# Optimization experiments

Hardware: AMD Instinct MI355X
Metric: run time of the kernel (lower is better)

The kernel has to match this reference:

```python
import jax, jax.numpy as jnp
import numpy as np

T = 8192   # sequence length (= max_seq_len)
E = 1024   # embedding dim
D = 11     # hard-coded projection dim in source


def setup_inputs() -> dict:
    key = jax.random.key(0)
    ks = jax.random.split(key, 6)
    s_e = 1.0 / np.sqrt(E)
    s_d = 1.0 / np.sqrt(D)
    return {
        "x": jax.random.randint(ks[0], (T,), 0, 32000, dtype=jnp.int64),
        "x_embeddings": jax.random.normal(ks[1], (T, E), dtype=jnp.float32),
        "Wk": jax.random.normal(ks[2], (D, E), dtype=jnp.float32) * s_e,
        "bk": jnp.zeros((D,), dtype=jnp.float32),
        "Wq": jax.random.normal(ks[3], (D, E), dtype=jnp.float32) * s_e,
        "bq": jnp.zeros((D,), dtype=jnp.float32),
        "Wv": jax.random.normal(ks[4], (D, E), dtype=jnp.float32) * s_e,
        "bv": jnp.zeros((D,), dtype=jnp.float32),
        "Wf": jax.random.normal(ks[5], (E, D), dtype=jnp.float32) * s_d,
        "bf": jnp.zeros((E,), dtype=jnp.float32),
    }


def reference(x, x_embeddings, Wk, bk, Wq, bq, Wv, bv, Wf, bf):
    t = x.shape[0]  # static under jit
    k = x_embeddings @ Wk.T + bk            # [T, D]
    q = x_embeddings @ Wq.T + bq            # [T, D]
    v = x_embeddings @ Wv.T + bv            # [T, D]
    att = q @ k.T                           # [T, T]; NOTE: no 1/sqrt(D) scaling in source
    causal = jnp.tril(jnp.ones((t, t), dtype=bool))
    att = jnp.where(causal, att, -jnp.inf)
    att = jax.nn.softmax(att, axis=1)       # dim=1 as in source
    res = att @ v                           # [T, D]
    return res @ Wf.T + bf                  # [T, E]
```

## Files before the change

kernel.cpp:

```cpp
#include <hip/hip_runtime.h>

#define T_SEQ 8192
#define E_DIM 1024
#define QS 36
#define QNEC 8
#define QKC 64
#define QX4 16
#define QXST 17
#define QRB 64
#define AJW 16
#define ABJ 64
#define ARB 256
#define KVW 24
#define TR 16

__device__ __forceinline__ float2 pkfma(float2 a, float2 b, float2 c) {
    return make_float2(fmaf(a.x, b.x, c.x), fmaf(a.y, b.y, c.y));
}
__device__ __forceinline__ float2 f2(float x, float y) { return make_float2(x, y); }

__device__ __forceinline__ void pack3s(const float2 o[6], float4* dst) {
    float4 t;
    t.x = o[0].x; t.y = o[0].y; t.z = o[1].x; t.w = o[1].y; dst[0]   = t;
    t.x = o[2].x; t.y = o[2].y; t.z = o[3].x; t.w = o[3].y; dst[64]  = t;
    t.x = o[4].x; t.y = o[4].y; t.z = o[5].x; t.w = o[5].y; dst[128] = t;
}
__device__ __forceinline__ void pack3(const float2 o[6], float4* dst) {
    float4 t;
    t.x = o[0].x; t.y = o[0].y; t.z = o[1].x; t.w = o[1].y; dst[0] = t;
    t.x = o[2].x; t.y = o[2].y; t.z = o[3].x; t.w = o[3].y; dst[1] = t;
    t.x = o[4].x; t.y = o[4].y; t.z = o[5].x; t.w = o[5].y; dst[2] = t;
}
__device__ __forceinline__ void add3s(float2 o[6], const float4* src) {
    float4 s0 = src[0], s1 = src[64], s2 = src[128];
    o[0].x += s0.x; o[0].y += s0.y; o[1].x += s0.z; o[1].y += s0.w;
    o[2].x += s1.x; o[2].y += s1.y; o[3].x += s1.z; o[3].y += s1.w;
    o[4].x += s2.x; o[4].y += s2.y; o[5].x += s2.z; o[5].y += s2.w;
}


__global__ __launch_bounds__(256) void qkv_proj(
    const float* __restrict__ xe,
    const float* __restrict__ Wk, const float* __restrict__ bk,
    const float* __restrict__ Wq, const float* __restrict__ bq,
    const float* __restrict__ Wv, const float* __restrict__ bv,
    float* __restrict__ partQ) {
    const int row0 = blockIdx.x * QRB;
    const int ec = blockIdx.y;
    const int lane = threadIdx.x & 63;
    const int wg = threadIdx.x >> 6;

    __shared__ float4 xT[QRB * QXST];
    __shared__ float4 wT[36 * QX4];

    float2 acc[9];
#pragma unroll
    for (int k = 0; k < 9; ++k) acc[k] = f2(0.f, 0.f);

    for (int cc = 0; cc < 2; ++cc) {
        const int cb = ec * 128 + cc * QKC;
        if (cc) __syncthreads();

#pragma unroll
        for (int t = 0; t < 4; ++t) {
            int idx = threadIdx.x + t * 256;
            int r = idx >> 4, c4 = idx & 15;
            xT[r * QXST + c4] =
                *(const float4*)(xe + (size_t)(row0 + r) * E_DIM + cb + c4 * 4);
        }
        for (int idx = threadIdx.x; idx < 36 * QX4; idx += 256) {
            int r = idx >> 4, c4 = idx & 15;
            float4 v = make_float4(0.f, 0.f, 0.f, 0.f);
            if (r < 33) {
                const float* base = (r < 11) ? (Wk + (size_t)r * E_DIM)
                                  : (r < 22) ? (Wq + (size_t)(r - 11) * E_DIM)
                                             : (Wv + (size_t)(r - 22) * E_DIM);
                v = *(const float4*)(base + cb + c4 * 4);
            }
            wT[idx] = v;
        }
        __syncthreads();

        const float4* xr = xT + lane * QXST;
        const float4* wr = wT + wg * 9 * QX4;
#pragma unroll 4
        for (int c4 = 0; c4 < QX4; ++c4) {
            float4 xv = xr[c4];
#pragma unroll
            for (int k = 0; k < 9; ++k) {
                float4 wv = wr[k * QX4 + c4];
                acc[k] = pkfma(f2(xv.x, xv.y), f2(wv.x, wv.y), acc[k]);
                acc[k] = pkfma(f2(xv.z, xv.w), f2(wv.z, wv.w), acc[k]);
            }
        }
    }

    __syncthreads();
    float* res = (float*)xT;
#pragma unroll
    for (int k = 0; k < 9; ++k) {
        int o = wg * 9 + k;
        bool live = (o < 33);
        int c = (o < 11) ? o : (o < 22) ? o + 1 : (o < 33) ? o + 2
              : (o == 33) ? 11 : (o == 34) ? 23 : 35;
        float b = 0.f;
        if (ec == 0 && live)
            b = (o < 11) ? bk[o] : (o < 22) ? bq[o - 11] : bv[o - 22];
        res[lane * 36 + c] = live ? (acc[k].x + acc[k].y + b) : 0.f;
    }
    __syncthreads();

    float4* dst = (float4*)(partQ + ((size_t)ec * T_SEQ + row0) * QS);
    for (int idx = threadIdx.x; idx < QRB * 9; idx += 256) {
        int r = idx / 9, f = idx % 9;
        dst[idx] = *(const float4*)(res + r * 36 + f * 4);
    }
}

__global__ __launch_bounds__(256) void reduceQ(const float* __restrict__ partQ,
                                               float* __restrict__ qkvF) {
    const size_t idx = (size_t)blockIdx.x * 256 + threadIdx.x;
    const float4* p = (const float4*)partQ;
    const size_t cs = (size_t)T_SEQ * (QS / 4);
    float4 s = make_float4(0.f, 0.f, 0.f, 0.f);
#pragma unroll
    for (int c = 0; c < QNEC; ++c) {
        float4 a = p[idx + (size_t)c * cs];
        s.x += a.x; s.y += a.y; s.z += a.z; s.w += a.w;
    }
    ((float4*)qkvF)[idx] = s;
}

__global__ __launch_bounds__(256) void attn(const float* __restrict__ qkvF,
                                            float* __restrict__ part) {
    const int b = blockIdx.x;
    int rb = 0;
    while (2 * (rb + 1) * (rb + 2) <= b) ++rb;
    const int c = b - 2 * rb * (rb + 1);
    const int lane = threadIdx.x & 63;
    const int wid = threadIdx.x >> 6;
    const int r0 = rb * ARB + lane * 4;
    const int j0 = c * ABJ + wid * AJW;

    __shared__ float sh[3072];
    float* kv = sh + wid * (AJW * KVW);

    float2 q[4][6], o[4][6];
#pragma unroll
    for (int i = 0; i < 4; ++i) {
        const float* qp = qkvF + (size_t)(r0 + i) * QS + 12;
#pragma unroll
        for (int d = 0; d < 5; ++d) q[i][d] = f2(qp[2 * d], qp[2 * d + 1]);
        q[i][5] = f2(qp[10], 0.f);
#pragma unroll
        for (int d = 0; d < 6; ++d) o[i][d] = f2(0.f, 0.f);
    }

#pragma unroll
    for (int t = 0; t < 2; ++t) {
        int idx = lane + t * 64;
        if (idx < AJW * 6) {
            int row = idx / 6, f = idx % 6;
            int srcOff = f * 4 + (f >= 3 ? 12 : 0);
            float4 v = *(const float4*)(qkvF + (size_t)(j0 + row) * QS + srcOff);
            *(float4*)(kv + row * KVW + f * 4) = v;
        }
    }

    for (int jj = 0; jj < AJW; ++jj) {
        const float* kp = kv + jj * KVW;
        const float4 kA = *(const float4*)(kp);
        const float4 kB = *(const float4*)(kp + 4);
        const float4 kC = *(const float4*)(kp + 8);
        const float4 vA = *(const float4*)(kp + 12);
        const float4 vB = *(const float4*)(kp + 16);
        const float4 vC = *(const float4*)(kp + 20);
        const float2 k01 = f2(kA.x, kA.y), k23 = f2(kA.z, kA.w);
        const float2 k45 = f2(kB.x, kB.y), k67 = f2(kB.z, kB.w);
        const float2 k89 = f2(kC.x, kC.y), kXp = f2(kC.z, kC.w);
        const int j = j0 + jj;

#pragma unroll
        for (int i = 0; i < 4; ++i) {
            float2 s = pkfma(q[i][0], k01, pkfma(q[i][1], k23, pkfma(q[i][2], k45,
                       pkfma(q[i][3], k67, pkfma(q[i][4], k89,
                       pkfma(q[i][5], kXp, f2(0.f, 0.f)))))));
            float pe = __expf(s.x + s.y);
            pe = (j <= r0 + i) ? pe : 0.f;
            float2 p2 = f2(pe, pe);
            o[i][0] = pkfma(p2, f2(vA.x, vA.y), o[i][0]);
            o[i][1] = pkfma(p2, f2(vA.z, vA.w), o[i][1]);
            o[i][2] = pkfma(p2, f2(vB.x, vB.y), o[i][2]);
            o[i][3] = pkfma(p2, f2(vB.z, vB.w), o[i][3]);
            o[i][4] = pkfma(p2, f2(vC.x, vC.y), o[i][4]);
            o[i][5] = pkfma(p2, f2(vC.z, 1.f),  o[i][5]);
        }
    }

    float4* buf = (float4*)sh;
    __syncthreads();
    if (wid == 1) {
#pragma unroll
        for (int i = 0; i < 4; ++i) pack3s(o[i], buf + (i * 3) * 64 + lane);
    }
    __syncthreads();
    if (wid == 0) {
#pragma unroll
        for (int i = 0; i < 4; ++i) add3s(o[i], buf + (i * 3) * 64 + lane);
    }
    __syncthreads();
    if (wid == 3) {
#pragma unroll
        for (int i = 0; i < 4; ++i) pack3s(o[i], buf + (i * 3) * 64 + lane);
    }
    __syncthreads();
    if (wid == 2) {
#pragma unroll
        for (int i = 0; i < 4; ++i) add3s(o[i], buf + (i * 3) * 64 + lane);
    }
    __syncthreads();
    if (wid == 2) {
#pragma unroll
        for (int i = 0; i < 4; ++i) pack3s(o[i], buf + (i * 3) * 64 + lane);
    }
    __syncthreads();
    if (wid == 0) {
#pragma unroll
        for (int i = 0; i < 4; ++i) add3s(o[i], buf + (i * 3) * 64 + lane);
        float* d0 = part + ((size_t)c * T_SEQ + r0) * 12;
#pragma unroll
        for (int i = 0; i < 4; ++i) pack3(o[i], (float4*)(d0 + i * 12));
    }
}

__global__ __launch_bounds__(256) void pass2(const float* __restrict__ part,
                                             const float* __restrict__ Wf,
                                             const float* __restrict__ bf,
                                             float* __restrict__ out) {
    const int t0 = blockIdx.x * TR;
    const int cnt = 4 * (t0 / ARB) + 4;
    __shared__ float red[16][16][12];
    __shared__ float res[TR][12];
    {
        const int r = threadIdx.x >> 4;
        const int s = threadIdx.x & 15;
        float a[12];
#pragma unroll
        for (int d = 0; d < 12; ++d) a[d] = 0.f;
        const size_t S = (size_t)T_SEQ * 12;
        const float* p = part + (size_t)(t0 + r) * 12;
        for (int c = s; c < cnt; c += 16) {
            const float4* pc = (const float4*)(p + (size_t)c * S);
            float4 x0 = pc[0], x1 = pc[1], x2 = pc[2];
            a[0] += x0.x; a[1] += x0.y; a[2]  += x0.z; a[3]  += x0.w;
            a[4] += x1.x; a[5] += x1.y; a[6]  += x1.z; a[7]  += x1.w;
            a[8] += x2.x; a[9] += x2.y; a[10] += x2.z; a[11] += x2.w;
        }
#pragma unroll
        for (int d = 0; d < 12; ++d) red[r][s][d] = a[d];
    }
    __syncthreads();
    if (threadIdx.x < TR * 12) {
        const int r = threadIdx.x / 12, d = threadIdx.x % 12;
        float sum = 0.f;
#pragma unroll
        for (int s = 0; s < 16; ++s) sum += red[r][s][d];
        res[r][d] = (d == 11) ? (1.f / sum) : sum;
    }
    __syncthreads();

    const int e0 = threadIdx.x * 4;
    float w[4][11];
    const float* wp = Wf + (size_t)e0 * 11;
#pragma unroll
    for (int ee = 0; ee < 4; ++ee)
#pragma unroll
        for (int i = 0; i < 11; ++i) w[ee][i] = wp[ee * 11 + i];
    const float4 bv = *(const float4*)(bf + e0);

    for (int r = 0; r < TR; ++r) {
        float rr[12];
#pragma unroll
        for (int d = 0; d < 12; ++d) rr[d] = res[r][d];
        float2 a0 = f2(0.f, 0.f), a1 = a0, a2 = a0, a3 = a0;
#pragma unroll
        for (int d = 0; d < 10; d += 2) {
            float2 rv = f2(rr[d], rr[d + 1]);
            a0 = pkfma(rv, f2(w[0][d], w[0][d + 1]), a0);
            a1 = pkfma(rv, f2(w[1][d], w[1][d + 1]), a1);
            a2 = pkfma(rv, f2(w[2][d], w[2][d + 1]), a2);
            a3 = pkfma(rv, f2(w[3][d], w[3][d + 1]), a3);
        }
        const float rl = rr[11];
        float4 ov;
        ov.x = (a0.x + a0.y + rr[10] * w[0][10]) * rl + bv.x;
        ov.y = (a1.x + a1.y + rr[10] * w[1][10]) * rl + bv.y;
        ov.z = (a2.x + a2.y + rr[10] * w[2][10]) * rl + bv.z;
        ov.w = (a3.x + a3.y + rr[10] * w[3][10]) * rl + bv.w;
        *(float4*)(out + (size_t)(t0 + r) * E_DIM + e0) = ov;
    }
}

extern "C" void kernel_launch(void* const* d_in, const int* in_sizes, int n_in,
                              void* d_out, int out_size, void* d_ws, size_t ws_size,
                              hipStream_t stream) {
    const float* xe = (const float*)d_in[1];
    const float* Wk = (const float*)d_in[2];
    const float* bk = (const float*)d_in[3];
    const float* Wq = (const float*)d_in[4];
    const float* bq = (const float*)d_in[5];
    const float* Wv = (const float*)d_in[6];
    const float* bv = (const float*)d_in[7];
    const float* Wf = (const float*)d_in[8];
    const float* bf = (const float*)d_in[9];
    float* out = (float*)d_out;

    float* qkvF  = (float*)d_ws;
    float* partQ = qkvF + (size_t)T_SEQ * QS;
    float* part  = partQ;

    qkv_proj<<<dim3(T_SEQ / QRB, QNEC), 256, 0, stream>>>(xe, Wk, bk, Wq, bq, Wv, bv, partQ);
    reduceQ<<<(T_SEQ * QS / 4) / 256, 256, 0, stream>>>(partQ, qkvF);
    attn<<<2112, 256, 0, stream>>>(qkvF, part);
    pass2<<<T_SEQ / TR, 256, 0, stream>>>(part, Wf, bf, out);
}
```

Before: 163.8 us.

## Fuse Q reduction into projection via last-block atomic and fold final attention row-block

```diff
diff --git a/kernel.cpp b/kernel.cpp
--- a/kernel.cpp
+++ b/kernel.cpp
@@ -44,7 +44,8 @@
     const float* __restrict__ Wk, const float* __restrict__ bk,
     const float* __restrict__ Wq, const float* __restrict__ bq,
     const float* __restrict__ Wv, const float* __restrict__ bv,
-    float* __restrict__ partQ) {
+    float* __restrict__ partQ, float* __restrict__ qkvF,
+    int* __restrict__ cntQ) {
     const int row0 = blockIdx.x * QRB;
     const int ec = blockIdx.y;
     const int lane = threadIdx.x & 63;
@@ -115,20 +116,27 @@
         int r = idx / 9, f = idx % 9;
         dst[idx] = *(const float4*)(res + r * 36 + f * 4);
     }
-}
-
-__global__ __launch_bounds__(256) void reduceQ(const float* __restrict__ partQ,
-                                               float* __restrict__ qkvF) {
-    const size_t idx = (size_t)blockIdx.x * 256 + threadIdx.x;
-    const float4* p = (const float4*)partQ;
-    const size_t cs = (size_t)T_SEQ * (QS / 4);
-    float4 s = make_float4(0.f, 0.f, 0.f, 0.f);
-#pragma unroll
-    for (int c = 0; c < QNEC; ++c) {
-        float4 a = p[idx + (size_t)c * cs];
-        s.x += a.x; s.y += a.y; s.z += a.z; s.w += a.w;
-    }
-    ((float4*)qkvF)[idx] = s;
+
+    __threadfence();
+    __shared__ int last;
+    if (threadIdx.x == 0)
+        last = (atomicAdd(&cntQ[blockIdx.x], 1) == QNEC - 1);
+    __syncthreads();
+    if (last) {
+        __threadfence();
+        const float4* p = (const float4*)(partQ + (size_t)row0 * QS);
+        const size_t cs = (size_t)T_SEQ * 9;
+        float4* q4 = (float4*)(qkvF + (size_t)row0 * QS);
+        for (int idx = threadIdx.x; idx < QRB * 9; idx += 256) {
+            float4 s = make_float4(0.f, 0.f, 0.f, 0.f);
+#pragma unroll
+            for (int cch = 0; cch < QNEC; ++cch) {
+                float4 a = p[(size_t)cch * cs + idx];
+                s.x += a.x; s.y += a.y; s.z += a.z; s.w += a.w;
+            }
+            q4[idx] = s;
+        }
+    }
 }
 
 __global__ __launch_bounds__(256) void attn(const float* __restrict__ qkvF,
@@ -140,7 +148,6 @@
     const int lane = threadIdx.x & 63;
     const int wid = threadIdx.x >> 6;
     const int r0 = rb * ARB + lane * 4;
-    const int j0 = c * ABJ + wid * AJW;
 
     __shared__ float sh[3072];
     float* kv = sh + wid * (AJW * KVW);
@@ -156,44 +163,51 @@
         for (int d = 0; d < 6; ++d) o[i][d] = f2(0.f, 0.f);
     }
 
-#pragma unroll
-    for (int t = 0; t < 2; ++t) {
-        int idx = lane + t * 64;
-        if (idx < AJW * 6) {
-            int row = idx / 6, f = idx % 6;
-            int srcOff = f * 4 + (f >= 3 ? 12 : 0);
-            float4 v = *(const float4*)(qkvF + (size_t)(j0 + row) * QS + srcOff);
-            *(float4*)(kv + row * KVW + f * 4) = v;
-        }
-    }
-
-    for (int jj = 0; jj < AJW; ++jj) {
-        const float* kp = kv + jj * KVW;
-        const float4 kA = *(const float4*)(kp);
-        const float4 kB = *(const float4*)(kp + 4);
-        const float4 kC = *(const float4*)(kp + 8);
-        const float4 vA = *(const float4*)(kp + 12);
-        const float4 vB = *(const float4*)(kp + 16);
-        const float4 vC = *(const float4*)(kp + 20);
-        const float2 k01 = f2(kA.x, kA.y), k23 = f2(kA.z, kA.w);
-        const float2 k45 = f2(kB.x, kB.y), k67 = f2(kB.z, kB.w);
-        const float2 k89 = f2(kC.x, kC.y), kXp = f2(kC.z, kC.w);
-        const int j = j0 + jj;
-
-#pragma unroll
-        for (int i = 0; i < 4; ++i) {
-            float2 s = pkfma(q[i][0], k01, pkfma(q[i][1], k23, pkfma(q[i][2], k45,
-                       pkfma(q[i][3], k67, pkfma(q[i][4], k89,
-                       pkfma(q[i][5], kXp, f2(0.f, 0.f)))))));
-            float pe = __expf(s.x + s.y);
-            pe = (j <= r0 + i) ? pe : 0.f;
-            float2 p2 = f2(pe, pe);
-            o[i][0] = pkfma(p2, f2(vA.x, vA.y), o[i][0]);
-            o[i][1] = pkfma(p2, f2(vA.z, vA.w), o[i][1]);
-            o[i][2] = pkfma(p2, f2(vB.x, vB.y), o[i][2]);
-            o[i][3] = pkfma(p2, f2(vB.z, vB.w), o[i][3]);
-            o[i][4] = pkfma(p2, f2(vC.x, vC.y), o[i][4]);
-            o[i][5] = pkfma(p2, f2(vC.z, 1.f),  o[i][5]);
+    const int npass = (rb == 31) ? 2 : 1;
+    for (int ps = 0; ps < npass; ++ps) {
+        const int jc = ps ? (127 - c) : c;
+        const int j0 = jc * ABJ + wid * AJW;
+        if (ps) __syncthreads();
+
+#pragma unroll
+        for (int t = 0; t < 2; ++t) {
+            int idx = lane + t * 64;
+            if (idx < AJW * 6) {
+                int row = idx / 6, f = idx % 6;
+                int srcOff = f * 4 + (f >= 3 ? 12 : 0);
+                float4 v = *(const float4*)(qkvF + (size_t)(j0 + row) * QS + srcOff);
+                *(float4*)(kv + row * KVW + f * 4) = v;
+            }
+        }
+
+        for (int jj = 0; jj < AJW; ++jj) {
+            const float* kp = kv + jj * KVW;
+            const float4 kA = *(const float4*)(kp);
+            const float4 kB = *(const float4*)(kp + 4);
+            const float4 kC = *(const float4*)(kp + 8);
+            const float4 vA = *(const float4*)(kp + 12);
+            const float4 vB = *(const float4*)(kp + 16);
+            const float4 vC = *(const float4*)(kp + 20);
+            const float2 k01 = f2(kA.x, kA.y), k23 = f2(kA.z, kA.w);
+            const float2 k45 = f2(kB.x, kB.y), k67 = f2(kB.z, kB.w);
+            const float2 k89 = f2(kC.x, kC.y), kXp = f2(kC.z, kC.w);
+            const int j = j0 + jj;
+
+#pragma unroll
+            for (int i = 0; i < 4; ++i) {
+                float2 s = pkfma(q[i][0], k01, pkfma(q[i][1], k23, pkfma(q[i][2], k45,
+                           pkfma(q[i][3], k67, pkfma(q[i][4], k89,
+                           pkfma(q[i][5], kXp, f2(0.f, 0.f)))))));
+                float pe = __expf(s.x + s.y);
+                pe = (j <= r0 + i) ? pe : 0.f;
+                float2 p2 = f2(pe, pe);
+                o[i][0] = pkfma(p2, f2(vA.x, vA.y), o[i][0]);
+                o[i][1] = pkfma(p2, f2(vA.z, vA.w), o[i][1]);
+                o[i][2] = pkfma(p2, f2(vB.x, vB.y), o[i][2]);
+                o[i][3] = pkfma(p2, f2(vB.z, vB.w), o[i][3]);
+                o[i][4] = pkfma(p2, f2(vC.x, vC.y), o[i][4]);
+                o[i][5] = pkfma(p2, f2(vC.z, 1.f),  o[i][5]);
+            }
         }
     }
 
@@ -238,7 +252,8 @@
                                              const float* __restrict__ bf,
                                              float* __restrict__ out) {
     const int t0 = blockIdx.x * TR;
-    const int cnt = 4 * (t0 / ARB) + 4;
+    const int g = t0 / ARB;
+    const int cnt = (g == 31) ? 64 : 4 * g + 4;
     __shared__ float red[16][16][12];
     __shared__ float res[TR][12];
     {
@@ -318,9 +333,11 @@
     float* qkvF  = (float*)d_ws;
     float* partQ = qkvF + (size_t)T_SEQ * QS;
     float* part  = partQ;
-
-    qkv_proj<<<dim3(T_SEQ / QRB, QNEC), 256, 0, stream>>>(xe, Wk, bk, Wq, bq, Wv, bv, partQ);
-    reduceQ<<<(T_SEQ * QS / 4) / 256, 256, 0, stream>>>(partQ, qkvF);
-    attn<<<2112, 256, 0, stream>>>(qkvF, part);
+    int*   cntQ  = (int*)(qkvF + (size_t)16 * 1024 * 1024);
+
+    hipMemsetAsync(cntQ, 0, 128 * sizeof(int), stream);
+    qkv_proj<<<dim3(T_SEQ / QRB, QNEC), 256, 0, stream>>>(xe, Wk, bk, Wq, bq, Wv, bv,
+                                                          partQ, qkvF, cntQ);
+    attn<<<2048, 256, 0, stream>>>(qkvF, part);
     pass2<<<T_SEQ / TR, 256, 0, stream>>>(part, Wf, bf, out);
 }
```

After: 275.1 us. 67.9% more time.
